# Optimization experiments

Measured on AMD Instinct MI355X. Metric: run time of the kernel, lower is better.

## Reference

```python
import jax, jax.numpy as jnp
import numpy as np

N_LAYERS = 4
N_EMBD = 1024
D_INNER = 2048
D_STATE = 16
DT_RANK = 64
D_CONV = 4
VOCAB = 50257
L = 2048
EPS = 1e-6


def setup_inputs() -> dict:
    key = jax.random.key(0)
    ks = jax.random.split(key, 8)
    s = 0.02
    tokens = jax.random.randint(ks[0], (L,), 0, VOCAB)
    emb_W = jax.random.normal(ks[1], (VOCAB, N_EMBD), jnp.float32) * s
    in_proj_W = jax.random.normal(ks[2], (N_LAYERS, 2 * D_INNER, N_EMBD), jnp.float32) * s
    conv_W = jax.random.normal(ks[3], (N_LAYERS, D_INNER, 1, D_CONV), jnp.float32) * 0.3
    conv_b = jnp.zeros((N_LAYERS, D_INNER), jnp.float32)
    xproj_W = jax.random.normal(ks[4], (N_LAYERS, DT_RANK + 2 * D_STATE, D_INNER), jnp.float32) * s
    dt_W = jax.random.normal(ks[5], (N_LAYERS, D_INNER, DT_RANK), jnp.float32) * s
    dt_b = jnp.zeros((N_LAYERS, D_INNER), jnp.float32)
    # A init exactly as in source: repeat(1..d_state, d_inner).reshape(d_inner, d_state)
    A = jnp.repeat(jnp.arange(1, D_STATE + 1), D_INNER).reshape(D_INNER, D_STATE).astype(jnp.float32)
    A_log = jnp.tile(jnp.log(A)[None], (N_LAYERS, 1, 1))
    Dp = jnp.ones((N_LAYERS, D_INNER), jnp.float32)
    out_W = jax.random.normal(ks[6], (N_LAYERS, N_EMBD, D_INNER), jnp.float32) * s
    rms_w = jnp.ones((N_LAYERS, N_EMBD), jnp.float32)
    rms_b = jnp.zeros((N_LAYERS, N_EMBD), jnp.float32)
    normf_w = jnp.ones((N_EMBD,), jnp.float32)
    normf_b = jnp.zeros((N_EMBD,), jnp.float32)
    return dict(tokens=tokens, emb_W=emb_W, in_proj_W=in_proj_W, conv_W=conv_W,
                conv_b=conv_b, xproj_W=xproj_W, dt_W=dt_W, dt_b=dt_b,
                A_log=A_log, Dp=Dp, out_W=out_W, rms_w=rms_w, rms_b=rms_b,
                normf_w=normf_w, normf_b=normf_b)


def _rmsnorm(x, w, b):
    inv = jax.lax.rsqrt(jnp.mean(x * x, axis=-1, keepdims=True) + EPS)
    return x * inv * w + b


def _selective_scan(u, delta, A, B, C, D):
    # u, delta: [L, d_inner]; A: [d_inner, d_state]; B, C: [L, d_state]
    dA = jnp.exp(jnp.einsum('ld,dn->ldn', delta, A))          # [L, d, n]
    dBu = jnp.einsum('ld,ln,ld->ldn', delta, B, u)            # [L, d, n]

    def step(s, inp):
        dA_t, dBu_t, C_t = inp
        s = dA_t * s + dBu_t                                  # [d, n]
        return s, s @ C_t                                     # y_t: [d]

    s0 = jnp.zeros((D_INNER, D_STATE), u.dtype)
    _, ys = jax.lax.scan(step, s0, (dA, dBu, C))
    return ys + u * D


def _forward(tokens, emb_W, in_proj_W, conv_W, conv_b, xproj_W, dt_W, dt_b,
             A_log, Dp, out_W, rms_w, rms_b, normf_w, normf_b):
    x = emb_W[tokens]                                          # [L, n_embd]
    for i in range(N_LAYERS):
        h = _rmsnorm(x, rms_w[i], rms_b[i])
        xr = h @ in_proj_W[i].T                                # [L, 2*d_inner]
        xc, res = jnp.split(xr, 2, axis=-1)
        # depthwise causal conv: pad d_conv-1 both sides, keep first L
        u = xc.T[None]                                         # [1, d_inner, L]
        u = jax.lax.conv_general_dilated(
            u, conv_W[i], window_strides=(1,),
            padding=[(D_CONV - 1, D_CONV - 1)],
            feature_group_count=D_INNER)[0, :, :L].T + conv_b[i]
        xc = jax.nn.silu(u)
        x_dbl = xc @ xproj_W[i].T                              # [L, dt_rank + 2*d_state]
        delta, B, C = jnp.split(x_dbl, [DT_RANK, DT_RANK + D_STATE], axis=-1)
        delta = jax.nn.softplus(delta @ dt_W[i].T + dt_b[i])   # [L, d_inner]
        y = _selective_scan(xc, delta, -jnp.exp(A_log[i]), B, C, Dp[i])
        y = y * jax.nn.silu(res)
        x = x + y @ out_W[i].T
    x = _rmsnorm(x, normf_w, normf_b)
    return x @ emb_W.T                                         # tied lm head [L, vocab]


def reference(tokens, emb_W, in_proj_W, conv_W, conv_b, xproj_W, dt_W, dt_b,
              A_log, Dp, out_W, rms_w, rms_b, normf_w, normf_b):
    return _forward(tokens, emb_W, in_proj_W, conv_W, conv_b, xproj_W, dt_W,
                    dt_b, A_log, Dp, out_W, rms_w, rms_b, normf_w, normf_b)
```

## Files before the change

kernel.cpp:

```cpp
#include <hip/hip_runtime.h>
#include <math.h>

#define L_SEQ   2048
#define NEMBD   1024
#define DINNER  2048
#define DSTATE  16
#define DTRANK  64
#define DCONV   4
#define VOCAB   50257
#define NLAYERS 4

__device__ __forceinline__ float silu_f(float x) { return x / (1.f + __expf(-x)); }
__device__ __forceinline__ float softplus_f(float x) { return x > 20.f ? x : log1pf(__expf(x)); }

__global__ void embed_k(const int* __restrict__ tok, const float* __restrict__ W,
                        float* __restrict__ x) {
    int idx = blockIdx.x * 256 + threadIdx.x;
    int l = idx >> 10, e = idx & 1023;
    x[idx] = W[(size_t)tok[l] * NEMBD + e];
}

__global__ void rmsnorm_k(const float* __restrict__ x, const float* __restrict__ w,
                          const float* __restrict__ b, float* __restrict__ o) {
    int l = blockIdx.x;
    const float* xr = x + (size_t)l * NEMBD;
    float ss = 0.f;
    for (int i = threadIdx.x; i < NEMBD; i += 256) { float v = xr[i]; ss += v * v; }
    __shared__ float red[4];
    for (int off = 32; off > 0; off >>= 1) ss += __shfl_down(ss, off, 64);
    if ((threadIdx.x & 63) == 0) red[threadIdx.x >> 6] = ss;
    __syncthreads();
    if (threadIdx.x == 0) {
        float t = red[0] + red[1] + red[2] + red[3];
        red[0] = rsqrtf(t / (float)NEMBD + 1e-6f);
    }
    __syncthreads();
    float inv = red[0];
    for (int i = threadIdx.x; i < NEMBD; i += 256)
        o[(size_t)l * NEMBD + i] = xr[i] * inv * w[i] + b[i];
}

__global__ void conv_silu_k(const float* __restrict__ xr, const float* __restrict__ cw,
                            const float* __restrict__ cb, float* __restrict__ xc) {
    int idx = blockIdx.x * 256 + threadIdx.x;
    int d = idx & (DINNER - 1); int l = idx >> 11;
    const float* w = cw + (size_t)d * DCONV;
    float acc = cb[d];
#pragma unroll
    for (int j = 0; j < DCONV; j++) {
        int t = l - (DCONV - 1) + j;
        if (t >= 0) acc = fmaf(xr[(size_t)t * (2 * DINNER) + d], w[j], acc);
    }
    xc[idx] = silu_f(acc);
}

__global__ void zero_k(float* __restrict__ p, int n) {
    int i = blockIdx.x * 256 + threadIdx.x;
    if (i < n) p[i] = 0.f;
}

#define BM 128
#define BN 128
#define BK 16
template <int EPI>
__global__ __launch_bounds__(256) void gemm_bt(
    const float* __restrict__ A, int lda,
    const float* __restrict__ B, int ldb,
    float* __restrict__ C, int ldc,
    const float* __restrict__ bias,
    int M, int N, int K, int nyt) {
    __shared__ __align__(16) float As[BK][BM + 4];
    __shared__ __align__(16) float Bs[BK][BN + 4];
    int tid = threadIdx.x;
    int bid = blockIdx.x;
    int bm = (bid % nyt) * BM;
    int bn = (bid / nyt) * BN;
    int Kc = K / (int)gridDim.y;
    int kb = blockIdx.y * Kc;
    int ke = kb + Kc;

    int sr = tid >> 2;
    int sc = (tid & 3) << 2;
    const float* Ap0 = A + (size_t)(bm + sr) * lda + sc;
    const float* Ap1 = Ap0 + (size_t)64 * lda;
    int br0 = bn + sr;      if (br0 > N - 1) br0 = N - 1;
    int br1 = bn + 64 + sr; if (br1 > N - 1) br1 = N - 1;
    const float* Bp0 = B + (size_t)br0 * ldb + sc;
    const float* Bp1 = B + (size_t)br1 * ldb + sc;

    float4 a0 = *(const float4*)(Ap0 + kb);
    float4 a1 = *(const float4*)(Ap1 + kb);
    float4 b0 = *(const float4*)(Bp0 + kb);
    float4 b1 = *(const float4*)(Bp1 + kb);

    int tx4 = (tid & 15) << 2;
    int ty4 = (tid >> 4) << 2;
    float acc[8][8] = {};

    for (int k0 = kb; k0 < ke; k0 += BK) {
        As[sc + 0][sr] = a0.x; As[sc + 1][sr] = a0.y;
        As[sc + 2][sr] = a0.z; As[sc + 3][sr] = a0.w;
        As[sc + 0][64 + sr] = a1.x; As[sc + 1][64 + sr] = a1.y;
        As[sc + 2][64 + sr] = a1.z; As[sc + 3][64 + sr] = a1.w;
        Bs[sc + 0][sr] = b0.x; Bs[sc + 1][sr] = b0.y;
        Bs[sc + 2][sr] = b0.z; Bs[sc + 3][sr] = b0.w;
        Bs[sc + 0][64 + sr] = b1.x; Bs[sc + 1][64 + sr] = b1.y;
        Bs[sc + 2][64 + sr] = b1.z; Bs[sc + 3][64 + sr] = b1.w;
        __syncthreads();
        if (k0 + BK < ke) {
            a0 = *(const float4*)(Ap0 + k0 + BK);
            a1 = *(const float4*)(Ap1 + k0 + BK);
            b0 = *(const float4*)(Bp0 + k0 + BK);
            b1 = *(const float4*)(Bp1 + k0 + BK);
        }
#pragma unroll
        for (int k = 0; k < BK; k++) {
            float4 av0 = *(const float4*)&As[k][ty4];
            float4 av1 = *(const float4*)&As[k][64 + ty4];
            float4 bv0 = *(const float4*)&Bs[k][tx4];
            float4 bv1 = *(const float4*)&Bs[k][64 + tx4];
            float av[8] = {av0.x, av0.y, av0.z, av0.w, av1.x, av1.y, av1.z, av1.w};
            float bv[8] = {bv0.x, bv0.y, bv0.z, bv0.w, bv1.x, bv1.y, bv1.z, bv1.w};
#pragma unroll
            for (int i = 0; i < 8; i++)
#pragma unroll
                for (int j = 0; j < 8; j++)
                    acc[i][j] = fmaf(av[i], bv[j], acc[i][j]);
        }
        __syncthreads();
    }

#pragma unroll
    for (int i = 0; i < 8; i++) {
        int gm = bm + (i < 4 ? ty4 + i : 64 + ty4 + i - 4);
#pragma unroll
        for (int j = 0; j < 8; j++) {
            int gn = bn + (j < 4 ? tx4 + j : 64 + tx4 + j - 4);
            if (gn >= N) continue;
            float v = acc[i][j];
            size_t off = (size_t)gm * ldc + gn;
            if (EPI == 0) C[off] = v;
            if (EPI == 1) C[off] = softplus_f(v + bias[gn]);
            if (EPI == 3) atomicAdd(&C[off], v);
        }
    }
}

__global__ __launch_bounds__(64) void scan_k(
    const float* __restrict__ xc, const float* __restrict__ delta,
    const float* __restrict__ xdbl, const float* __restrict__ Alog,
    const float* __restrict__ Dpv, const float* __restrict__ xr,
    float* __restrict__ y) {
    int gid = blockIdx.x * 64 + threadIdx.x;
    int d = gid >> 4;
    int n = gid & 15;
    float a = -__expf(Alog[(size_t)d * DSTATE + n]);
    float Dd = Dpv[d];
    float s = 0.f;

    float dA[8], uA[8], BA[8], CA[8], rA[8];
    float dB[8], uB[8], BB[8], CB[8], rB[8];

#define LOADG(DL, UU, BV, CV, RR, lbase)                              \
    _Pragma("unroll")                                                 \
    for (int j = 0; j < 8; j++) {                                     \
        int ll = (lbase) + j; if (ll > L_SEQ - 1) ll = L_SEQ - 1;     \
        DL[j] = delta[(size_t)ll * DINNER + d];                       \
        UU[j] = xc[(size_t)ll * DINNER + d];                          \
        BV[j] = xdbl[(size_t)ll * 96 + DTRANK + n];                   \
        CV[j] = xdbl[(size_t)ll * 96 + DTRANK + DSTATE + n];          \
        RR[j] = xr[(size_t)ll * (2 * DINNER) + DINNER + d];           \
    }

#define STEP8(DL, UU, BV, CV, RR, lbase)                              \
    _Pragma("unroll")                                                 \
    for (int j = 0; j < 8; j++) {                                     \
        float e = __expf(DL[j] * a);                                  \
        s = fmaf(e, s, DL[j] * UU[j] * BV[j]);                        \
        float p = s * CV[j];                                          \
        p += __shfl_xor(p, 1, 64);                                    \
        p += __shfl_xor(p, 2, 64);                                    \
        p += __shfl_xor(p, 4, 64);                                    \
        p += __shfl_xor(p, 8, 64);                                    \
        if (n == 0)                                                   \
            y[(size_t)((lbase) + j) * DINNER + d] =                   \
                fmaf(UU[j], Dd, p) * silu_f(RR[j]);                   \
    }

    LOADG(dA, uA, BA, CA, rA, 0)
    for (int l0 = 0; l0 < L_SEQ; l0 += 16) {
        LOADG(dB, uB, BB, CB, rB, l0 + 8)
        STEP8(dA, uA, BA, CA, rA, l0)
        LOADG(dA, uA, BA, CA, rA, l0 + 16)
        STEP8(dB, uB, BB, CB, rB, l0 + 8)
    }
#undef LOADG
#undef STEP8
}

extern "C" void kernel_launch(void* const* d_in, const int* in_sizes, int n_in,
                              void* d_out, int out_size, void* d_ws, size_t ws_size,
                              hipStream_t stream) {
    (void)in_sizes; (void)n_in; (void)out_size; (void)ws_size;
    const int*   tokens    = (const int*)d_in[0];
    const float* emb_W     = (const float*)d_in[1];
    const float* in_proj_W = (const float*)d_in[2];
    const float* conv_W    = (const float*)d_in[3];
    const float* conv_b    = (const float*)d_in[4];
    const float* xproj_W   = (const float*)d_in[5];
    const float* dt_W      = (const float*)d_in[6];
    const float* dt_b      = (const float*)d_in[7];
    const float* A_log     = (const float*)d_in[8];
    const float* Dp        = (const float*)d_in[9];
    const float* out_W     = (const float*)d_in[10];
    const float* rms_w     = (const float*)d_in[11];
    const float* rms_b     = (const float*)d_in[12];
    const float* normf_w   = (const float*)d_in[13];
    const float* normf_b   = (const float*)d_in[14];
    float* out = (float*)d_out;

    float* ws   = (float*)d_ws;
    float* x    = ws;
    float* h    = x    + (size_t)L_SEQ * NEMBD;
    float* xr   = h    + (size_t)L_SEQ * NEMBD;
    float* xc   = xr   + (size_t)L_SEQ * 2 * DINNER;
    float* xdbl = xc   + (size_t)L_SEQ * DINNER;
    float* dlt  = xdbl + (size_t)L_SEQ * 96;
    float* y    = dlt  + (size_t)L_SEQ * DINNER;

    dim3 blk(256);

    embed_k<<<(L_SEQ * NEMBD) / 256, blk, 0, stream>>>(tokens, emb_W, x);

    for (int i = 0; i < NLAYERS; i++) {
        const float* ipW = in_proj_W + (size_t)i * 2 * DINNER * NEMBD;
        const float* cW  = conv_W   + (size_t)i * DINNER * DCONV;
        const float* cB  = conv_b   + (size_t)i * DINNER;
        const float* xpW = xproj_W  + (size_t)i * 96 * DINNER;
        const float* dW  = dt_W     + (size_t)i * DINNER * DTRANK;
        const float* dB  = dt_b     + (size_t)i * DINNER;
        const float* Al  = A_log    + (size_t)i * DINNER * DSTATE;
        const float* Dl  = Dp       + (size_t)i * DINNER;
        const float* oW  = out_W    + (size_t)i * NEMBD * DINNER;

        rmsnorm_k<<<L_SEQ, blk, 0, stream>>>(x, rms_w + (size_t)i * NEMBD,
                                             rms_b + (size_t)i * NEMBD, h);
        gemm_bt<0><<<dim3(32 * 16, 1), blk, 0, stream>>>(
            h, NEMBD, ipW, NEMBD, xr, 2 * DINNER, nullptr,
            L_SEQ, 2 * DINNER, NEMBD, 16);
        conv_silu_k<<<(L_SEQ * DINNER) / 256, blk, 0, stream>>>(xr, cW, cB, xc);
        zero_k<<<(L_SEQ * 96) / 256, blk, 0, stream>>>(xdbl, L_SEQ * 96);
        gemm_bt<3><<<dim3(1 * 16, 8), blk, 0, stream>>>(
            xc, DINNER, xpW, DINNER, xdbl, 96, nullptr,
            L_SEQ, 96, DINNER, 16);
        gemm_bt<1><<<dim3(16 * 16, 1), blk, 0, stream>>>(
            xdbl, 96, dW, DTRANK, dlt, DINNER, dB,
            L_SEQ, DINNER, DTRANK, 16);
        scan_k<<<(DINNER * DSTATE) / 64, dim3(64), 0, stream>>>(
            xc, dlt, xdbl, Al, Dl, xr, y);
        gemm_bt<3><<<dim3(8 * 16, 2), blk, 0, stream>>>(
            y, DINNER, oW, DINNER, x, NEMBD, nullptr,
            L_SEQ, NEMBD, DINNER, 16);
    }

    rmsnorm_k<<<L_SEQ, blk, 0, stream>>>(x, normf_w, normf_b, h);
    gemm_bt<0><<<dim3(393 * 16, 1), blk, 0, stream>>>(
        h, NEMBD, emb_W, NEMBD, out, VOCAB, nullptr,
        L_SEQ, VOCAB, NEMBD, 16);
}
```

Baseline: 6.996 ms.

## Run LM head GEMM in fp16 with MFMA instead of fp32 SIMT

Adds a kernel that converts emb_W and the final normed activations to fp16, then a 128x128x64 MFMA GEMM (16x16x32 f16) with swizzled LDS and register prefetch computes the vocab logits. The path is used only when the workspace is large enough; otherwise it falls back to the fp32 GEMM. The goal is to replace the dominant fp32 vocab-projection GEMM with matrix-core throughput. In exchange it converts the full embedding matrix on every call and loses precision by using fp16 inputs.

```diff
diff --git a/kernel.cpp b/kernel.cpp
--- a/kernel.cpp
+++ b/kernel.cpp
@@ -9,6 +9,10 @@
 #define DCONV   4
 #define VOCAB   50257
 #define NLAYERS 4
+#define VOCAB_PAD 50304
+
+typedef _Float16 f16x8 __attribute__((ext_vector_type(8)));
+typedef float f32x4 __attribute__((ext_vector_type(4)));
 
 __device__ __forceinline__ float silu_f(float x) { return x / (1.f + __expf(-x)); }
 __device__ __forceinline__ float softplus_f(float x) { return x > 20.f ? x : log1pf(__expf(x)); }
@@ -57,6 +61,110 @@
 __global__ void zero_k(float* __restrict__ p, int n) {
     int i = blockIdx.x * 256 + threadIdx.x;
     if (i < n) p[i] = 0.f;
+}
+
+__global__ void cvt_f16_k(const float* __restrict__ s, unsigned short* __restrict__ d,
+                          int n8) {
+    int i = blockIdx.x * 256 + threadIdx.x;
+    if (i >= n8) return;
+    float4 v0 = ((const float4*)s)[(size_t)i * 2];
+    float4 v1 = ((const float4*)s)[(size_t)i * 2 + 1];
+    union { _Float16 h[8]; uint4 u; } r;
+    r.h[0] = (_Float16)v0.x; r.h[1] = (_Float16)v0.y;
+    r.h[2] = (_Float16)v0.z; r.h[3] = (_Float16)v0.w;
+    r.h[4] = (_Float16)v1.x; r.h[5] = (_Float16)v1.y;
+    r.h[6] = (_Float16)v1.z; r.h[7] = (_Float16)v1.w;
+    ((uint4*)d)[i] = r.u;
+}
+
+__global__ __launch_bounds__(256) void gemm_f16(
+    const unsigned short* __restrict__ A, int lda,
+    const unsigned short* __restrict__ B, int ldb,
+    float* __restrict__ C, int ldc,
+    int N, int K, int mtiles) {
+    __shared__ unsigned short As[128 * 64];
+    __shared__ unsigned short Bs[128 * 64];
+    int bid = blockIdx.x;
+    int bm = (bid % mtiles) << 7;
+    int bn = (bid / mtiles) << 7;
+    int tid = threadIdx.x;
+    int lane = tid & 63;
+    int wc = (tid >> 6) & 1;
+    int wr = tid >> 7;
+
+    int srow = tid >> 3;
+    int kcol = (tid & 7) << 3;
+    int swoff = (((tid & 7) ^ ((tid >> 3) & 7)) << 3);
+    const unsigned short* Ab = A + (size_t)(bm + srow) * lda + kcol;
+    const unsigned short* Bb = B + (size_t)(bn + srow) * ldb + kcol;
+    unsigned short* AsW = As + srow * 64 + swoff;
+    unsigned short* BsW = Bs + srow * 64 + swoff;
+
+    uint4 ra[4], rb[4];
+#pragma unroll
+    for (int i = 0; i < 4; i++) {
+        ra[i] = *(const uint4*)(Ab + (size_t)(i * 32) * lda);
+        rb[i] = *(const uint4*)(Bb + (size_t)(i * 32) * ldb);
+    }
+
+    int q = lane >> 4;
+    int fr = lane & 15;
+    f32x4 acc[4][4] = {};
+
+    int nk = K >> 6;
+    for (int kt = 0; kt < nk; kt++) {
+        __syncthreads();
+#pragma unroll
+        for (int i = 0; i < 4; i++) {
+            *(uint4*)(AsW + i * (32 * 64)) = ra[i];
+            *(uint4*)(BsW + i * (32 * 64)) = rb[i];
+        }
+        __syncthreads();
+        if (kt + 1 < nk) {
+            int k0 = (kt + 1) << 6;
+#pragma unroll
+            for (int i = 0; i < 4; i++) {
+                ra[i] = *(const uint4*)(Ab + (size_t)(i * 32) * lda + k0);
+                rb[i] = *(const uint4*)(Bb + (size_t)(i * 32) * ldb + k0);
+            }
+        }
+#pragma unroll
+        for (int kk = 0; kk < 2; kk++) {
+            f16x8 af[4], bf[4];
+#pragma unroll
+            for (int mf = 0; mf < 4; mf++) {
+                int row = wr * 64 + mf * 16 + fr;
+                int ch = (kk * 4 + q) ^ (row & 7);
+                af[mf] = *(const f16x8*)(As + row * 64 + ch * 8);
+            }
+#pragma unroll
+            for (int nf = 0; nf < 4; nf++) {
+                int row = wc * 64 + nf * 16 + fr;
+                int ch = (kk * 4 + q) ^ (row & 7);
+                bf[nf] = *(const f16x8*)(Bs + row * 64 + ch * 8);
+            }
+#pragma unroll
+            for (int mf = 0; mf < 4; mf++)
+#pragma unroll
+                for (int nf = 0; nf < 4; nf++)
+                    acc[mf][nf] = __builtin_amdgcn_mfma_f32_16x16x32_f16(
+                        af[mf], bf[nf], acc[mf][nf], 0, 0, 0);
+        }
+    }
+
+    int crow0 = bm + wr * 64 + (lane >> 4) * 4;
+    int ccol0 = bn + wc * 64 + (lane & 15);
+#pragma unroll
+    for (int mf = 0; mf < 4; mf++)
+#pragma unroll
+        for (int nf = 0; nf < 4; nf++) {
+            int gcol = ccol0 + nf * 16;
+            if (gcol >= N) continue;
+            float* cp = C + (size_t)(crow0 + mf * 16) * ldc + gcol;
+#pragma unroll
+            for (int r = 0; r < 4; r++)
+                cp[(size_t)r * ldc] = acc[mf][nf][r];
+        }
 }
 
 #define BM 128
@@ -201,7 +309,7 @@
 extern "C" void kernel_launch(void* const* d_in, const int* in_sizes, int n_in,
                               void* d_out, int out_size, void* d_ws, size_t ws_size,
                               hipStream_t stream) {
-    (void)in_sizes; (void)n_in; (void)out_size; (void)ws_size;
+    (void)in_sizes; (void)n_in; (void)out_size;
     const int*   tokens    = (const int*)d_in[0];
     const float* emb_W     = (const float*)d_in[1];
     const float* in_proj_W = (const float*)d_in[2];
@@ -227,6 +335,12 @@
     float* xdbl = xc   + (size_t)L_SEQ * DINNER;
     float* dlt  = xdbl + (size_t)L_SEQ * 96;
     float* y    = dlt  + (size_t)L_SEQ * DINNER;
+
+    size_t f32_elems = (size_t)L_SEQ * (2 * NEMBD + 2 * DINNER + DINNER + 96 + DINNER + DINNER);
+    unsigned short* embH = (unsigned short*)(ws + f32_elems);
+    unsigned short* hH   = embH + (size_t)VOCAB_PAD * NEMBD;
+    size_t need = f32_elems * 4 + (size_t)VOCAB_PAD * NEMBD * 2 + (size_t)L_SEQ * NEMBD * 2;
+    bool use_f16_head = (ws_size >= need);
 
     dim3 blk(256);
 
@@ -264,7 +378,18 @@
     }
 
     rmsnorm_k<<<L_SEQ, blk, 0, stream>>>(x, normf_w, normf_b, h);
-    gemm_bt<0><<<dim3(393 * 16, 1), blk, 0, stream>>>(
-        h, NEMBD, emb_W, NEMBD, out, VOCAB, nullptr,
-        L_SEQ, VOCAB, NEMBD, 16);
-}
+    if (use_f16_head) {
+        zero_k<<<(((VOCAB_PAD - VOCAB) * NEMBD / 2) + 255) / 256, blk, 0, stream>>>(
+            (float*)(embH + (size_t)VOCAB * NEMBD), (VOCAB_PAD - VOCAB) * NEMBD / 2);
+        int n8e = VOCAB * NEMBD / 8;
+        cvt_f16_k<<<(n8e + 255) / 256, blk, 0, stream>>>(emb_W, embH, n8e);
+        int n8h = L_SEQ * NEMBD / 8;
+        cvt_f16_k<<<(n8h + 255) / 256, blk, 0, stream>>>(h, hH, n8h);
+        gemm_f16<<<dim3((VOCAB_PAD / 128) * 16), blk, 0, stream>>>(
+            hH, NEMBD, embH, NEMBD, out, VOCAB, VOCAB, NEMBD, 16);
+    } else {
+        gemm_bt<0><<<dim3(393 * 16, 1), blk, 0, stream>>>(
+            h, NEMBD, emb_W, NEMBD, out, VOCAB, nullptr,
+            L_SEQ, VOCAB, NEMBD, 16);
+    }
+}
```

Result: faster. 5.845 ms (-16.5%).
